# Kernel optimization log

Measured on AMD Instinct MI355X. Metric: run time of the kernel, lower is better.

The kernel has to match this reference:

```python
import jax, jax.numpy as jnp
import numpy as np

NUM_GROUPS = 32
EPS = 1e-6


def setup_inputs() -> dict:
    key = jax.random.key(0)
    ks = jax.random.split(key, 10)
    B, C, L = 8, 512, 4096
    s = 1.0 / np.sqrt(C)
    x = jax.random.normal(ks[0], (B, C, L), dtype=jnp.float32)
    gn_w = jnp.ones((C,), jnp.float32)
    gn_b = jnp.zeros((C,), jnp.float32)
    wq = jax.random.normal(ks[1], (C, C), jnp.float32) * s
    bq = jax.random.normal(ks[2], (C,), jnp.float32) * 0.01
    wk = jax.random.normal(ks[3], (C, C), jnp.float32) * s
    bk = jax.random.normal(ks[4], (C,), jnp.float32) * 0.01
    wv = jax.random.normal(ks[5], (C, C), jnp.float32) * s
    bv = jax.random.normal(ks[6], (C,), jnp.float32) * 0.01
    wo = jax.random.normal(ks[7], (C, C), jnp.float32) * s
    bo = jax.random.normal(ks[8], (C,), jnp.float32) * 0.01
    return {"x": x, "gn_w": gn_w, "gn_b": gn_b, "wq": wq, "bq": bq,
            "wk": wk, "bk": bk, "wv": wv, "bv": bv, "wo": wo, "bo": bo}


def _group_norm(x, w, b):
    # x: [B, C, L]; normalize over each group's (C/G, L) slice
    B, C, L = x.shape
    g = x.reshape(B, NUM_GROUPS, C // NUM_GROUPS, L)
    mu = jnp.mean(g, axis=(2, 3), keepdims=True)
    var = jnp.var(g, axis=(2, 3), keepdims=True)
    g = (g - mu) * jax.lax.rsqrt(var + EPS)
    return g.reshape(B, C, L) * w[None, :, None] + b[None, :, None]


def _conv1x1(h, w, b):
    # pointwise conv: [B,C,L] x [Cout,Cin] -> [B,Cout,L]
    return jnp.einsum('oc,bcl->bol', w, h) + b[None, :, None]


def reference(x, gn_w, gn_b, wq, bq, wk, bk, wv, bv, wo, bo):
    h = _group_norm(x, gn_w, gn_b)
    q = _conv1x1(h, wq, bq)
    k = _conv1x1(h, wk, bk)
    v = _conv1x1(h, wv, bv)
    B, C, L = q.shape
    scale = jnp.asarray(C, q.dtype) ** -0.5
    # w_[b,i,j] = sum_c q[b,c,i] k[b,c,j]
    w_ = jnp.einsum('bci,bcj->bij', q, k) * scale
    w_ = jax.nn.softmax(w_, axis=2)
    # h[b,c,i] = sum_j v[b,c,j] w_[b,i,j]
    h = jnp.einsum('bcj,bij->bci', v, w_)
    return x + _conv1x1(h, wo, bo)
```

## Files before the change

kernel.cpp:

```cpp
#include <hip/hip_runtime.h>
#include <hip/hip_bf16.h>
#include <math.h>

#define DI __device__ __forceinline__

typedef unsigned short u16;
typedef unsigned int   u32;
typedef unsigned long long u64;
typedef __attribute__((ext_vector_type(8))) short short8;
typedef __attribute__((ext_vector_type(4))) float f32x4;

constexpr int CB = 512;
constexpr int LL = 4096;
constexpr int NG = 32;
constexpr long NELC = (long)LL * CB;

DI float bf2f(u16 u) { u32 v = ((u32)u) << 16; float f; __builtin_memcpy(&f, &v, 4); return f; }
DI u16 f2bf(float f) {
  u32 u; __builtin_memcpy(&u, &f, 4);
  u += 0x7fffu + ((u >> 16) & 1u);
  return (u16)(u >> 16);
}

DI void gload16(const void* g, void* l) {
  __builtin_amdgcn_global_load_lds((const __attribute__((address_space(1))) u32*)g,
                                   (__attribute__((address_space(3))) u32*)l, 16, 0, 0);
}

__global__ __launch_bounds__(256) void conv_w(
    const float* __restrict__ wq, const float* __restrict__ wk,
    const float* __restrict__ wv, const float* __restrict__ wo,
    const float* __restrict__ bq, const float* __restrict__ bk,
    const float* __restrict__ bv,
    u16* __restrict__ wqkv, u16* __restrict__ wob, float* __restrict__ bqkv) {
  if (blockIdx.x < 1024) {
    int i = blockIdx.x * 256 + threadIdx.x;
    wqkv[i]          = f2bf(wq[i]);
    wqkv[262144 + i] = f2bf(wk[i]);
    wqkv[524288 + i] = f2bf(wv[i]);
    wob[i]           = f2bf(wo[i]);
  } else {
    for (int j = 0; j < 6; ++j) {
      int idx = j * 256 + threadIdx.x;
      float b = (idx < 512) ? bq[idx] : (idx < 1024) ? bk[idx - 512] : bv[idx - 1024];
      bqkv[idx] = b;
    }
  }
}

__global__ __launch_bounds__(256) void gn_stats(const float* __restrict__ x,
                                                float* __restrict__ stats) {
  const float4* base = (const float4*)(x + (long)blockIdx.x * (16 * LL));
  float s = 0.f, ss = 0.f;
  for (int i = threadIdx.x; i < 16 * LL / 4; i += 256) {
    float4 v = base[i];
    s  += v.x + v.y + v.z + v.w;
    ss += v.x * v.x + v.y * v.y + v.z * v.z + v.w * v.w;
  }
#pragma unroll
  for (int o = 32; o; o >>= 1) { s += __shfl_xor(s, o); ss += __shfl_xor(ss, o); }
  __shared__ float red[8];
  int wv = threadIdx.x >> 6, ln = threadIdx.x & 63;
  if (ln == 0) { red[wv * 2] = s; red[wv * 2 + 1] = ss; }
  __syncthreads();
  if (threadIdx.x == 0) {
    float S = red[0] + red[2] + red[4] + red[6];
    float SS = red[1] + red[3] + red[5] + red[7];
    float mu = S * (1.f / 65536.f);
    float var = SS * (1.f / 65536.f) - mu * mu;
    stats[blockIdx.x * 2]     = mu;
    stats[blockIdx.x * 2 + 1] = rsqrtf(var + 1e-6f);
  }
}

__global__ __launch_bounds__(256) void gn_apply(
    const float* __restrict__ x, const float* __restrict__ gw,
    const float* __restrict__ gb, const float* __restrict__ stats,
    u16* __restrict__ hT) {
  __shared__ u16 t[64][66];
  const int b = blockIdx.z, c0 = blockIdx.y * 64, l0 = blockIdx.x * 64;
  const int ln = threadIdx.x & 63, sub = threadIdx.x >> 6;
  for (int cr = sub; cr < 64; cr += 4) {
    int c = c0 + cr;
    float v  = x[(long)b * CB * LL + (long)c * LL + l0 + ln];
    float mu = stats[(b * NG + (c >> 4)) * 2];
    float rs = stats[(b * NG + (c >> 4)) * 2 + 1];
    t[cr][ln] = f2bf((v - mu) * rs * gw[c] + gb[c]);
  }
  __syncthreads();
  for (int lr = sub; lr < 64; lr += 4)
    hT[(long)b * LL * CB + (long)(l0 + lr) * CB + c0 + ln] = t[ln][lr];
}

template <int Q>
DI void rdA(const u16* LB, int wr, int fr, int fq, short8 af[2][2]) {
#pragma unroll
  for (int m2 = 0; m2 < 2; ++m2)
#pragma unroll
    for (int kk = 0; kk < 2; ++kk) {
      const int R = wr * 128 + (Q * 2 + m2) * 16 + fr;
      af[m2][kk] = *(const short8*)((const char*)LB + R * 128 +
                                    ((kk * 64 + fq * 16) ^ ((R & 7) << 4)));
    }
}
DI void rdB(const u16* LB, int wc, int fr, int fq, short8 bf[4][2]) {
#pragma unroll
  for (int nf = 0; nf < 4; ++nf)
#pragma unroll
    for (int kk = 0; kk < 2; ++kk) {
      const int R = wc * 64 + nf * 16 + fr;
      bf[nf][kk] = *(const short8*)((const char*)LB + R * 128 +
                                    ((kk * 64 + fq * 16) ^ ((R & 7) << 4)));
    }
}
template <int Q>
DI void mmaQ(short8 af[2][2], short8 bf[4][2], f32x4 acc[8][4]) {
#pragma unroll
  for (int kk = 0; kk < 2; ++kk)
#pragma unroll
    for (int m2 = 0; m2 < 2; ++m2)
#pragma unroll
      for (int nf = 0; nf < 4; ++nf)
        acc[Q * 2 + m2][nf] = __builtin_amdgcn_mfma_f32_16x16x32_bf16(
            af[m2][kk], bf[nf][kk], acc[Q * 2 + m2][nf], 0, 0, 0);
}

#define PTAIL(Q)                                             \
  __builtin_amdgcn_s_barrier();                              \
  asm volatile("s_waitcnt lgkmcnt(0)" ::: "memory");         \
  __builtin_amdgcn_sched_barrier(0);                         \
  __builtin_amdgcn_s_setprio(1);                             \
  mmaQ<Q>(af, bf, acc);                                      \
  __builtin_amdgcn_s_setprio(0);                             \
  __builtin_amdgcn_s_barrier();

template <int EPI>
__global__ __launch_bounds__(512, 2) void gemm8p(
    const u16* __restrict__ A, int lda, long asb,
    const u16* __restrict__ Bt, int ldb, long bsb,
    int K, const float* __restrict__ bias, float scale,
    u16* __restrict__ o0, u16* __restrict__ o1, u16* __restrict__ o2,
    const float* __restrict__ rls, long osb, int ldo) {
  __shared__ u16 smem[65536];
  u16* lA0 = smem;
  u16* lA1 = smem + 16384;
  u16* lB0 = smem + 32768;
  u16* lB1 = smem + 49152;

  const int tid = threadIdx.x;
  const int lane = tid & 63, wv = tid >> 6;
  const int wr = wv >> 2, wc = wv & 3;
  const int fr = lane & 15, fq = lane >> 4;
  const int bx = blockIdx.x, by = blockIdx.y, bz = blockIdx.z;
  const int bzb = (EPI == 2) ? (bz >> 2) : bz;
  const int tb  = (EPI == 2) ? (bz & 3) * (K >> 6) : 0;

  const u16* Ab = A + (long)bzb * asb + (long)(by * 256) * lda;
  const u16* Bb = Bt + (long)bzb * bsb + (long)(bx * 256) * ldb;

  auto stage = [&](u16* lbase, const u16* gbase, int ld_, int half, int t) {
#pragma unroll
    for (int p = 0; p < 2; ++p) {
      int i = p * 512 + tid;
      int row = i >> 3, ch = i & 7;
      int src = t * 64 + ((((ch << 4) ^ ((row & 7) << 4))) >> 1);
      gload16(gbase + (long)(half * 128 + row) * ld_ + src,
              lbase + half * 8192 + i * 8);
    }
  };

  f32x4 acc[8][4];
#pragma unroll
  for (int m = 0; m < 8; ++m)
#pragma unroll
    for (int n = 0; n < 4; ++n) acc[m][n] = (f32x4)(0.f);

  stage(lA0, Ab, lda, 0, tb); stage(lA0, Ab, lda, 1, tb);
  stage(lB0, Bb, ldb, 0, tb); stage(lB0, Bb, ldb, 1, tb);
  stage(lB1, Bb, ldb, 0, tb + 1); stage(lB1, Bb, ldb, 1, tb + 1);
  asm volatile("s_waitcnt vmcnt(4)" ::: "memory");
  __builtin_amdgcn_sched_barrier(0);
  __builtin_amdgcn_s_barrier();

  const int nt = K >> 6;
  short8 af[2][2], bf[4][2];
  for (int i = 0; i < nt / 2; ++i) {
    const bool last = (i == nt / 2 - 1);
    const int t1 = tb + 2 * i + 1, t2 = tb + 2 * i + 2, t3 = tb + 2 * i + 3;
    rdB(lB0, wc, fr, fq, bf);
    rdA<0>(lA0, wr, fr, fq, af);
    stage(lA1, Ab, lda, 0, t1);
    PTAIL(0)
    rdA<1>(lA0, wr, fr, fq, af);
    stage(lA1, Ab, lda, 1, t1);
    PTAIL(1)
    rdA<2>(lA0, wr, fr, fq, af);
    if (!last) stage(lB0, Bb, ldb, 0, t2);
    PTAIL(2)
    rdA<3>(lA0, wr, fr, fq, af);
    if (!last) stage(lB0, Bb, ldb, 1, t2);
    if (last) { asm volatile("s_waitcnt vmcnt(0)" ::: "memory"); }
    else      { asm volatile("s_waitcnt vmcnt(4)" ::: "memory"); }
    __builtin_amdgcn_sched_barrier(0);
    PTAIL(3)
    rdB(lB1, wc, fr, fq, bf);
    rdA<0>(lA1, wr, fr, fq, af);
    if (!last) stage(lA0, Ab, lda, 0, t2);
    PTAIL(0)
    rdA<1>(lA1, wr, fr, fq, af);
    if (!last) stage(lA0, Ab, lda, 1, t2);
    PTAIL(1)
    rdA<2>(lA1, wr, fr, fq, af);
    if (!last) stage(lB1, Bb, ldb, 0, t3);
    PTAIL(2)
    rdA<3>(lA1, wr, fr, fq, af);
    if (!last) stage(lB1, Bb, ldb, 1, t3);
    if (!last) {
      asm volatile("s_waitcnt vmcnt(4)" ::: "memory");
      __builtin_amdgcn_sched_barrier(0);
    }
    PTAIL(3)
  }

  if constexpr (EPI == 1) {
#pragma unroll
    for (int mf = 0; mf < 8; ++mf)
#pragma unroll
      for (int nf = 0; nf < 4; ++nf) {
        const int nl = wc * 64 + nf * 16 + fr;
#pragma unroll
        for (int r = 0; r < 4; ++r) {
          const int ml = wr * 128 + mf * 16 + fq * 4 + r;
          smem[ml * 256 + (nl ^ ((ml & 7) << 3))] =
              f2bf(exp2f(acc[mf][nf][r] * scale));
        }
      }
    __syncthreads();
    u16* dst0 = o0 + (long)bz * osb + (long)(by * 256) * ldo + bx * 256;
    for (int i = tid * 8; i < 65536; i += 4096) {
      const int rr = i >> 8, cc = i & 255;
      short8 val = *(const short8*)&smem[rr * 256 + (cc ^ ((rr & 7) << 3))];
      *(short8*)(dst0 + (long)rr * ldo + cc) = val;
    }
  } else if constexpr (EPI == 2) {
    const float* rl = rls + (long)bzb * LL + by * 256;
#pragma unroll
    for (int mf = 0; mf < 8; ++mf)
#pragma unroll
      for (int nf = 0; nf < 4; ++nf) {
        const int nl = wc * 64 + nf * 16 + fr;
#pragma unroll
        for (int r = 0; r < 4; ++r) {
          const int ml = wr * 128 + mf * 16 + fq * 4 + r;
          smem[ml * 256 + (nl ^ ((ml & 7) << 3))] =
              f2bf(acc[mf][nf][r] * rl[ml]);
        }
      }
    __syncthreads();
    u16* dst0 = o0 + (long)bzb * 4 * NELC + (long)(by * 256) * 2048 +
                (bz & 3) * 512 + bx * 256;
    for (int i = tid * 8; i < 65536; i += 4096) {
      const int rr = i >> 8, cc = i & 255;
      short8 val = *(const short8*)&smem[rr * 256 + (cc ^ ((rr & 7) << 3))];
      *(short8*)(dst0 + (long)rr * 2048 + cc) = val;
    }
  } else {
    const int mat = by >> 1;
    if (mat < 2) {
#pragma unroll
      for (int mf = 0; mf < 8; ++mf)
#pragma unroll
        for (int nf = 0; nf < 4; ++nf) {
          const int nl = wc * 64 + nf * 16 + fr;
#pragma unroll
          for (int r = 0; r < 4; ++r) {
            const int ml = wr * 128 + mf * 16 + fq * 4 + r;
            smem[nl * 256 + (ml ^ ((nl & 7) << 3))] =
                f2bf(acc[mf][nf][r] + bias[by * 256 + ml]);
          }
        }
      __syncthreads();
      u16* dst0 = (mat == 0 ? o0 : o1) + (long)bz * NELC +
                  (long)(bx * 256) * CB + ((by * 256) & 511);
      for (int i = tid * 8; i < 65536; i += 4096) {
        const int rr = i >> 8, cc = i & 255;
        short8 val = *(const short8*)&smem[rr * 256 + (cc ^ ((rr & 7) << 3))];
        *(short8*)(dst0 + (long)rr * CB + cc) = val;
      }
    } else {
#pragma unroll
      for (int mf = 0; mf < 8; ++mf)
#pragma unroll
        for (int nf = 0; nf < 4; ++nf) {
          const int nl = wc * 64 + nf * 16 + fr;
#pragma unroll
          for (int r = 0; r < 4; ++r) {
            const int ml = wr * 128 + mf * 16 + fq * 4 + r;
            smem[ml * 256 + (nl ^ ((ml & 7) << 3))] =
                f2bf(acc[mf][nf][r] + bias[by * 256 + ml]);
          }
        }
      __syncthreads();
      u16* dst0 = o2 + (long)bz * ((long)CB * LL) +
                  (long)((by * 256) & 511) * LL + bx * 256;
      for (int i = tid * 8; i < 65536; i += 4096) {
        const int rr = i >> 8, cc = i & 255;
        short8 val = *(const short8*)&smem[rr * 256 + (cc ^ ((rr & 7) << 3))];
        *(short8*)(dst0 + (long)rr * LL + cc) = val;
      }
    }
  }
}

template <int BM, int BN, int EPI, bool SWZ, int WR, int WC>
__global__ __launch_bounds__(WR * WC * 64) void gemm_bt(
    const u16* __restrict__ A, int lda, long asb,
    const u16* __restrict__ Bt, int ldb, long bsb,
    int K, const float* __restrict__ bias, float scale,
    u16* __restrict__ o0, u16* __restrict__ o1, u16* __restrict__ o2,
    float* __restrict__ of, const float* __restrict__ xres, long osb, int ldo) {
  constexpr int NT = WR * WC * 64;
  constexpr int FM = BM / WR / 16, FN = BN / WC / 16;
  static_assert((BM * 8) % NT == 0 && (BN * 8) % NT == 0, "staging div");
  __shared__ u16 smem[(BM + BN) * 64];
  u16* lA = smem;
  u16* lB = smem + BM * 64;

  int bx = blockIdx.x, by = blockIdx.y;
  if constexpr (SWZ) {
    const int nwg = gridDim.x * gridDim.y;
    const int id = by * gridDim.x + bx;
    const int id2 = (id & 7) * (nwg >> 3) + (id >> 3);
    bx = id2 % gridDim.x;
    by = id2 / gridDim.x;
  }

  const int tid = threadIdx.x;
  const int lane = tid & 63;
  const int wv = tid >> 6;
  const int wr = wv / WC, wc = wv % WC;
  const int fr = lane & 15, fq = lane >> 4;
  const int bz = blockIdx.z;
  const int bzb  = (EPI == 4) ? (bz >> 1) : bz;
  const int kbeg = (EPI == 4) ? (bz & 1) * K : 0;

  const u16* Ab = A + (long)bzb * asb + (long)(by * BM) * lda;
  const u16* Bb = Bt + (long)bzb * bsb + (long)(bx * BN) * ldb;

  f32x4 acc[FM][FN];
#pragma unroll
  for (int m = 0; m < FM; ++m)
#pragma unroll
    for (int n = 0; n < FN; ++n) acc[m][n] = (f32x4)(0.f);

  for (int k0 = kbeg; k0 < kbeg + K; k0 += 64) {
#pragma unroll
    for (int p = 0; p < BM * 8 / NT; ++p) {
      int t = p * NT + tid;
      int row = t >> 3;
      int cbl = ((t & 7) << 4) ^ ((row & 7) << 4);
      gload16(Ab + (long)row * lda + k0 + (cbl >> 1), &lA[t * 8]);
    }
#pragma unroll
    for (int p = 0; p < BN * 8 / NT; ++p) {
      int t = p * NT + tid;
      int row = t >> 3;
      int cbl = ((t & 7) << 4) ^ ((row & 7) << 4);
      gload16(Bb + (long)row * ldb + k0 + (cbl >> 1), &lB[t * 8]);
    }
    __syncthreads();
#pragma unroll
    for (int ks = 0; ks < 2; ++ks) {
      short8 af[FM], bfr[FN];
#pragma unroll
      for (int m = 0; m < FM; ++m) {
        int row = wr * (BM / WR) + m * 16 + fr;
        int cb = (ks * 64 + fq * 16) ^ ((row & 7) << 4);
        af[m] = *(const short8*)((const char*)lA + row * 128 + cb);
      }
#pragma unroll
      for (int n = 0; n < FN; ++n) {
        int row = wc * (BN / WC) + n * 16 + fr;
        int cb = (ks * 64 + fq * 16) ^ ((row & 7) << 4);
        bfr[n] = *(const short8*)((const char*)lB + row * 128 + cb);
      }
#pragma unroll
      for (int m = 0; m < FM; ++m)
#pragma unroll
        for (int n = 0; n < FN; ++n)
          acc[m][n] = __builtin_amdgcn_mfma_f32_16x16x32_bf16(af[m], bfr[n], acc[m][n], 0, 0, 0);
    }
    __syncthreads();
  }

  const int ml0 = wr * (BM / WR);
  const int nl0 = wc * (BN / WC);

  if constexpr (EPI == 3) {
    const int mg0 = by * BM + ml0;
    const int ng0 = bx * BN + nl0;
#pragma unroll
    for (int m = 0; m < FM; ++m)
#pragma unroll
      for (int n = 0; n < FN; ++n) {
        const int ng = ng0 + n * 16 + fr;
#pragma unroll
        for (int r = 0; r < 4; ++r) {
          const int mg = mg0 + m * 16 + fq * 4 + r;
          const long off = (long)bz * osb + (long)mg * ldo + ng;
          of[off] = acc[m][n][r] + bias[mg] + xres[off];
        }
      }
  } else {
    const float* rls = xres + (long)(bz >> 1) * LL + by * BM;
#pragma unroll
    for (int m = 0; m < FM; ++m)
#pragma unroll
      for (int n = 0; n < FN; ++n) {
        const int nl = nl0 + n * 16 + fr;
#pragma unroll
        for (int r = 0; r < 4; ++r) {
          const int ml = ml0 + m * 16 + fq * 4 + r;
          smem[ml * BN + (nl ^ ((ml & 7) << 3))] = f2bf(acc[m][n][r] * rls[ml]);
        }
      }
    __syncthreads();
    u16* dst0 = ((bz & 1) ? o1 : o0) + (long)(bz >> 1) * NELC +
                (long)(by * BM) * ldo + bx * BN;
    for (int i = tid * 8; i < BM * BN; i += NT * 8) {
      const int rr = i / BN, cc = i % BN;
      short8 val = *(const short8*)&smem[rr * BN + (cc ^ ((rr & 7) << 3))];
      *(short8*)(dst0 + (long)rr * ldo + cc) = val;
    }
  }
}

__global__ __launch_bounds__(256) void rsum_rows(const u16* __restrict__ S,
                                                 float* __restrict__ rls) {
  const u16* row = S + ((long)blockIdx.y * LL + blockIdx.x) * LL;
  const int tid = threadIdx.x;
  const int wv = tid >> 6, ln = tid & 63;
  short8 a = ((const short8*)row)[tid * 2];
  short8 b = ((const short8*)row)[tid * 2 + 1];
  float s = 0.f;
#pragma unroll
  for (int j = 0; j < 8; ++j) s += bf2f((u16)a[j]) + bf2f((u16)b[j]);
#pragma unroll
  for (int o = 32; o; o >>= 1) s += __shfl_xor(s, o);
  __shared__ float red[4];
  if (ln == 0) red[wv] = s;
  __syncthreads();
  if (tid == 0)
    rls[(long)blockIdx.y * LL + blockIdx.x] =
        1.0f / (red[0] + red[1] + red[2] + red[3]);
}

__global__ __launch_bounds__(256) void reduce4(
    const u16* __restrict__ P, u16* __restrict__ o) {
  const int b = blockIdx.y;
  const long idx = (long)blockIdx.x * 256 + threadIdx.x;
  const int i = (int)(idx >> 6);
  const int c0 = ((int)idx & 63) * 8;
  const u16* Pb = P + (long)b * 4 * NELC + (long)i * 2048;
  float s[8] = {0.f, 0.f, 0.f, 0.f, 0.f, 0.f, 0.f, 0.f};
#pragma unroll
  for (int c4 = 0; c4 < 4; ++c4) {
    short8 v = *(const short8*)(Pb + c4 * 512 + c0);
#pragma unroll
    for (int j = 0; j < 8; ++j) s[j] += bf2f((u16)v[j]);
  }
  short8 r;
#pragma unroll
  for (int j = 0; j < 8; ++j) r[j] = (short)f2bf(s[j]);
  *(short8*)(o + (long)b * NELC + (long)i * 512 + c0) = r;
}

__global__ __launch_bounds__(256) void reduce_pp(
    const u16* __restrict__ p0, const u16* __restrict__ p1, u16* __restrict__ o) {
  const long base = (long)blockIdx.y * NELC +
                    (long)(blockIdx.x * 256 + threadIdx.x) * 16;
#pragma unroll
  for (int h = 0; h < 2; ++h) {
    short8 a = *(const short8*)(p0 + base + h * 8);
    short8 b = *(const short8*)(p1 + base + h * 8);
    short8 r;
#pragma unroll
    for (int j = 0; j < 8; ++j)
      r[j] = (short)f2bf(bf2f((u16)a[j]) + bf2f((u16)b[j]));
    *(short8*)(o + base + h * 8) = r;
  }
}

extern "C" void kernel_launch(void* const* d_in, const int* in_sizes, int n_in,
                              void* d_out, int out_size, void* d_ws, size_t ws_size,
                              hipStream_t stream) {
  const float* x   = (const float*)d_in[0];
  const float* gnw = (const float*)d_in[1];
  const float* gnb = (const float*)d_in[2];
  const float* wq  = (const float*)d_in[3];
  const float* bq  = (const float*)d_in[4];
  const float* wk  = (const float*)d_in[5];
  const float* bk  = (const float*)d_in[6];
  const float* wv  = (const float*)d_in[7];
  const float* bv  = (const float*)d_in[8];
  const float* wo  = (const float*)d_in[9];
  const float* bo  = (const float*)d_in[10];
  float* out = (float*)d_out;

  char* ws = (char*)d_ws;
  const long NEL = NELC;
  const long SEL = (long)LL * LL;
  float* stats = (float*)ws;
  float* bqkv  = (float*)(ws + 8192);
  u16* wqkv = (u16*)(ws + 16384);
  u16* wob  = (u16*)(ws + 16384 + 1572864);
  float* rlsm = (float*)(ws + (3l << 20));
  u16* hT   = (u16*)(ws + (4l << 20));
  u16* qT   = hT + 8 * NEL;
  u16* kT   = qT + 8 * NEL;
  u16* vN   = kT + 8 * NEL;
  const size_t base = (4ul << 20) + 4ul * 8 * NEL * 2;

  const int G = (ws_size >= base + 2ul * SEL * 2) ? 2 : 1;
  u16* Sbuf = (G == 2) ? (u16*)(ws + base) : hT;

  conv_w<<<1025, 256, 0, stream>>>(wq, wk, wv, wo, bq, bk, bv, wqkv, wob, bqkv);
  gn_stats<<<256, 256, 0, stream>>>(x, stats);
  gn_apply<<<dim3(64, 8, 8), 256, 0, stream>>>(x, gnw, gnb, stats, hT);

  gemm8p<0><<<dim3(16, 6, 8), 512, 0, stream>>>(
      wqkv, 512, 0, hT, 512, NEL, 512, bqkv, 1.f, qT, kT, vN, nullptr, 0, 0);

  const float cl = (1.0f / sqrtf(512.0f)) * 1.44269504f;
  for (int g0 = 0; g0 < 8; g0 += G) {
    gemm8p<1><<<dim3(16, 16, G), 512, 0, stream>>>(
        qT + (long)g0 * NEL, 512, NEL, kT + (long)g0 * NEL, 512, NEL, 512,
        nullptr, cl, Sbuf, nullptr, nullptr, nullptr, SEL, LL);
    rsum_rows<<<dim3(LL, G), 256, 0, stream>>>(Sbuf, rlsm);
    if (G == 2) {
      gemm8p<2><<<dim3(2, 16, 8), 512, 0, stream>>>(
          Sbuf, LL, SEL, vN + (long)g0 * NEL, LL, NEL, 1024,
          nullptr, 1.f, hT, nullptr, nullptr, rlsm, 0, 0);
      reduce4<<<dim3(1024, 2), 256, 0, stream>>>(hT, qT + (long)g0 * NEL);
    } else {
      gemm_bt<128, 128, 4, true, 2, 4><<<dim3(4, 32, 2), 512, 0, stream>>>(
          Sbuf, LL, SEL, vN + (long)g0 * NEL, LL, NEL, 2048,
          nullptr, 1.f, qT + (long)g0 * NEL, kT + (long)g0 * NEL, nullptr,
          nullptr, rlsm, 0, CB);
      reduce_pp<<<dim3(512, 1), 256, 0, stream>>>(
          qT + (long)g0 * NEL, kT + (long)g0 * NEL, qT + (long)g0 * NEL);
    }
  }

  gemm_bt<128, 128, 3, false, 2, 2><<<dim3(32, 4, 8), 256, 0, stream>>>(
      wob, 512, 0, qT, 512, NEL, 512, bo, 1.f,
      nullptr, nullptr, nullptr, out, x, NEL, LL);

  (void)in_sizes; (void)n_in; (void)out_size; (void)ws_size;
}
```

Baseline: 597.5 us.

## Fuse softmax row-sum partials into QK^T epilogue and remap PV block order

The QK^T GEMM epilogue now accumulates per-row partial sums of the exponentiated scores in fp32 and writes them to a small partials buffer. A tiny combine kernel then produces reciprocal row sums, replacing the kernel that re-read the whole bf16 score matrix. The PV GEMM also remaps block IDs so that blocks sharing data are scheduled together, which is meant to improve cache locality. Costs: extra shuffles in the epilogue, a larger workspace requirement, and sums now taken from fp32 values rather than rounded bf16 ones.

```diff
diff --git a/kernel.cpp b/kernel.cpp
--- a/kernel.cpp
+++ b/kernel.cpp
@@ -140,7 +140,8 @@
     const u16* __restrict__ Bt, int ldb, long bsb,
     int K, const float* __restrict__ bias, float scale,
     u16* __restrict__ o0, u16* __restrict__ o1, u16* __restrict__ o2,
-    const float* __restrict__ rls, long osb, int ldo) {
+    const float* __restrict__ rls, float* __restrict__ spp,
+    long osb, int ldo) {
   __shared__ u16 smem[65536];
   u16* lA0 = smem;
   u16* lA1 = smem + 16384;
@@ -151,7 +152,13 @@
   const int lane = tid & 63, wv = tid >> 6;
   const int wr = wv >> 2, wc = wv & 3;
   const int fr = lane & 15, fq = lane >> 4;
-  const int bx = blockIdx.x, by = blockIdx.y, bz = blockIdx.z;
+
+  int bx = blockIdx.x, by = blockIdx.y, bz = blockIdx.z;
+  if constexpr (EPI == 2) {
+    const int fid = blockIdx.x + 2 * (blockIdx.y + 16 * blockIdx.z);
+    const int lid = (fid & 7) * 32 + (fid >> 3);
+    bx = lid & 1; by = (lid >> 1) & 15; bz = lid >> 5;
+  }
   const int bzb = (EPI == 2) ? (bz >> 2) : bz;
   const int tb  = (EPI == 2) ? (bz & 3) * (K >> 6) : 0;
 
@@ -224,17 +231,29 @@
 
   if constexpr (EPI == 1) {
 #pragma unroll
-    for (int mf = 0; mf < 8; ++mf)
+    for (int mf = 0; mf < 8; ++mf) {
+      float rp4[4] = {0.f, 0.f, 0.f, 0.f};
 #pragma unroll
       for (int nf = 0; nf < 4; ++nf) {
         const int nl = wc * 64 + nf * 16 + fr;
 #pragma unroll
         for (int r = 0; r < 4; ++r) {
           const int ml = wr * 128 + mf * 16 + fq * 4 + r;
-          smem[ml * 256 + (nl ^ ((ml & 7) << 3))] =
-              f2bf(exp2f(acc[mf][nf][r] * scale));
+          float p = exp2f(acc[mf][nf][r] * scale);
+          rp4[r] += p;
+          smem[ml * 256 + (nl ^ ((ml & 7) << 3))] = f2bf(p);
         }
       }
+#pragma unroll
+      for (int r = 0; r < 4; ++r) {
+        float v = rp4[r];
+        v += __shfl_xor(v, 1); v += __shfl_xor(v, 2);
+        v += __shfl_xor(v, 4); v += __shfl_xor(v, 8);
+        if (fr == 0)
+          spp[((long)bz * 64 + bx * 4 + wc) * LL +
+              by * 256 + wr * 128 + mf * 16 + fq * 4 + r] = v;
+      }
+    }
     __syncthreads();
     u16* dst0 = o0 + (long)bz * osb + (long)(by * 256) * ldo + bx * 256;
     for (int i = tid * 8; i < 65536; i += 4096) {
@@ -435,24 +454,15 @@
   }
 }
 
-__global__ __launch_bounds__(256) void rsum_rows(const u16* __restrict__ S,
-                                                 float* __restrict__ rls) {
-  const u16* row = S + ((long)blockIdx.y * LL + blockIdx.x) * LL;
-  const int tid = threadIdx.x;
-  const int wv = tid >> 6, ln = tid & 63;
-  short8 a = ((const short8*)row)[tid * 2];
-  short8 b = ((const short8*)row)[tid * 2 + 1];
+__global__ __launch_bounds__(256) void rls_combine(const float* __restrict__ spp,
+                                                   float* __restrict__ rls) {
+  const int row = blockIdx.x * 256 + threadIdx.x;
+  const int z = blockIdx.y;
+  const float* b = spp + (long)z * 64 * LL + row;
   float s = 0.f;
 #pragma unroll
-  for (int j = 0; j < 8; ++j) s += bf2f((u16)a[j]) + bf2f((u16)b[j]);
-#pragma unroll
-  for (int o = 32; o; o >>= 1) s += __shfl_xor(s, o);
-  __shared__ float red[4];
-  if (ln == 0) red[wv] = s;
-  __syncthreads();
-  if (tid == 0)
-    rls[(long)blockIdx.y * LL + blockIdx.x] =
-        1.0f / (red[0] + red[1] + red[2] + red[3]);
+  for (int j = 0; j < 64; ++j) s += b[(long)j * LL];
+  rls[(long)z * LL + row] = 1.0f / s;
 }
 
 __global__ __launch_bounds__(256) void reduce4(
@@ -521,26 +531,30 @@
   u16* vN   = kT + 8 * NEL;
   const size_t base = (4ul << 20) + 4ul * 8 * NEL * 2;
 
-  const int G = (ws_size >= base + 2ul * SEL * 2) ? 2 : 1;
-  u16* Sbuf = (G == 2) ? (u16*)(ws + base) : hT;
+  const int G = (ws_size >= base + 2ul * SEL * 2 + (4ul << 20)) ? 2 : 1;
+  u16* Sbuf;
+  float* spp;
+  if (G == 2) { Sbuf = (u16*)(ws + base); spp = (float*)(ws + base + 2ul * SEL * 2); }
+  else        { Sbuf = hT;                spp = (float*)(ws + base); }
 
   conv_w<<<1025, 256, 0, stream>>>(wq, wk, wv, wo, bq, bk, bv, wqkv, wob, bqkv);
   gn_stats<<<256, 256, 0, stream>>>(x, stats);
   gn_apply<<<dim3(64, 8, 8), 256, 0, stream>>>(x, gnw, gnb, stats, hT);
 
   gemm8p<0><<<dim3(16, 6, 8), 512, 0, stream>>>(
-      wqkv, 512, 0, hT, 512, NEL, 512, bqkv, 1.f, qT, kT, vN, nullptr, 0, 0);
+      wqkv, 512, 0, hT, 512, NEL, 512, bqkv, 1.f, qT, kT, vN,
+      nullptr, nullptr, 0, 0);
 
   const float cl = (1.0f / sqrtf(512.0f)) * 1.44269504f;
   for (int g0 = 0; g0 < 8; g0 += G) {
     gemm8p<1><<<dim3(16, 16, G), 512, 0, stream>>>(
         qT + (long)g0 * NEL, 512, NEL, kT + (long)g0 * NEL, 512, NEL, 512,
-        nullptr, cl, Sbuf, nullptr, nullptr, nullptr, SEL, LL);
-    rsum_rows<<<dim3(LL, G), 256, 0, stream>>>(Sbuf, rlsm);
+        nullptr, cl, Sbuf, nullptr, nullptr, nullptr, spp, SEL, LL);
+    rls_combine<<<dim3(16, G), 256, 0, stream>>>(spp, rlsm);
     if (G == 2) {
       gemm8p<2><<<dim3(2, 16, 8), 512, 0, stream>>>(
           Sbuf, LL, SEL, vN + (long)g0 * NEL, LL, NEL, 1024,
-          nullptr, 1.f, hT, nullptr, nullptr, rlsm, 0, 0);
+          nullptr, 1.f, hT, nullptr, nullptr, rlsm, nullptr, 0, 0);
       reduce4<<<dim3(1024, 2), 256, 0, stream>>>(hT, qT + (long)g0 * NEL);
     } else {
       gemm_bt<128, 128, 4, true, 2, 4><<<dim3(4, 32, 2), 512, 0, stream>>>(
```

Result: slower. 658.0 us (+10.1%).
